# Optimization experiments

Measured on AMD Instinct MI355X. Metric: run time of the kernel, lower is better.

Reference implementation:

```python
import jax, jax.numpy as jnp
import numpy as np

C = 256
NH = 4  # attention heads
G = 8   # groupnorm groups
EPS = 1e-5


def group_norm(x, weight, bias):
    B, Cc, H, W = x.shape
    xg = x.reshape(B, G, Cc // G, H, W)
    mean = xg.mean(axis=(2, 3, 4), keepdims=True)
    var = xg.var(axis=(2, 3, 4), keepdims=True)
    xg = (xg - mean) * jax.lax.rsqrt(var + EPS)
    xn = xg.reshape(B, Cc, H, W)
    return xn * weight[None, :, None, None] + bias[None, :, None, None]


def setup_inputs() -> dict:
    key = jax.random.key(0)
    ks = jax.random.split(key, 7)
    B, H, W = 16, 32, 32
    x = jax.random.normal(ks[0], (B, C, H, W), dtype=jnp.float32)
    n_weight = jnp.ones((C,), dtype=jnp.float32)
    n_bias = jnp.zeros((C,), dtype=jnp.float32)
    qkv_w = jax.random.normal(ks[1], (3 * C, C), dtype=jnp.float32) * (C ** -0.5)
    qkv_b = jnp.zeros((3 * C,), dtype=jnp.float32)
    p_w = jax.random.normal(ks[2], (C, C), dtype=jnp.float32) * (C ** -0.5)
    p_b = jnp.zeros((C,), dtype=jnp.float32)
    return {"x": x, "n_weight": n_weight, "n_bias": n_bias,
            "qkv_w": qkv_w, "qkv_b": qkv_b, "p_w": p_w, "p_b": p_b}


def reference(x, n_weight, n_bias, qkv_w, qkv_b, p_w, p_b):
    B, Cc, H, W = x.shape
    N = H * W
    dh = Cc // NH
    sc = dh ** -0.5
    xn = group_norm(x, n_weight, n_bias)  # [B,C,H,W]
    xn_flat = xn.reshape(B, Cc, N)
    # 1x1 conv == channel matmul
    qkv = jnp.einsum('oc,bcn->bon', qkv_w, xn_flat) + qkv_b[None, :, None]
    qkv = qkv.reshape(B, 3, NH, dh, N)
    q, k, v = qkv[:, 0], qkv[:, 1], qkv[:, 2]  # [B,h,dh,N]
    a = jax.nn.softmax(jnp.einsum('bhci,bhcj->bhij', q, k) * sc, axis=-1)
    o = jnp.einsum('bhij,bhcj->bhci', a, v).reshape(B, Cc, N)
    proj = jnp.einsum('oc,bcn->bon', p_w, o) + p_b[None, :, None]
    return x + proj.reshape(B, Cc, H, W)
```

## Files before the change

kernel.cpp:

```cpp
#include <hip/hip_runtime.h>
#include <math.h>

typedef unsigned short ushort;
typedef unsigned int uint;
typedef __attribute__((ext_vector_type(8))) short bf16x8;
typedef __attribute__((ext_vector_type(4))) float f32x4;

constexpr int Bc  = 16;
constexpr float EPSc = 1e-5f;
constexpr float QSC  = 0.18033688f;

__device__ inline ushort f2bf(float f) {
    uint u = __float_as_uint(f);
    uint r = (u + 0x7fffu + ((u >> 16) & 1u)) >> 16;
    return (ushort)r;
}
__device__ inline uint pack2(float a, float b) {
    return (uint)f2bf(a) | ((uint)f2bf(b) << 16);
}
__device__ __forceinline__ uint cvt2(float a, float b) {
    uint r;
    asm("v_cvt_pk_bf16_f32 %0, %1, %2" : "=v"(r) : "v"(a), "v"(b));
    return r;
}
__device__ __forceinline__ ushort f2bf_fast(float f) {
    uint r;
    asm("v_cvt_pk_bf16_f32 %0, %1, %2" : "=v"(r) : "v"(f), "v"(f));
    return (ushort)r;
}
#if __has_builtin(__builtin_amdgcn_exp2f)
#define EXP2F(x) __builtin_amdgcn_exp2f(x)
#else
#define EXP2F(x) __expf((x) * 0.69314718f)
#endif
__device__ __forceinline__ void gl_lds16(const ushort* g, ushort* l) {
    __builtin_amdgcn_global_load_lds(
        (const __attribute__((address_space(1))) void*)g,
        (__attribute__((address_space(3))) void*)l, 16, 0, 0);
}

__global__ __launch_bounds__(256) void pre_k(
    const float* __restrict__ x, const float* __restrict__ qkvw,
    const float* __restrict__ pw, float* __restrict__ pstats,
    ushort* __restrict__ wqb, ushort* __restrict__ pwb) {
    int blk = blockIdx.x;
    if (blk < 512) {
        int bg = blk >> 2, part = blk & 3;
        const float4* p = (const float4*)(x + (size_t)bg * 32768 + part * 8192);
        float s = 0.f, s2 = 0.f;
        for (int i = threadIdx.x; i < 2048; i += 256) {
            float4 v = p[i];
            s += v.x + v.y + v.z + v.w;
            s2 += v.x*v.x + v.y*v.y + v.z*v.z + v.w*v.w;
        }
        __shared__ float rs[256], rq[256];
        rs[threadIdx.x] = s; rq[threadIdx.x] = s2;
        __syncthreads();
        for (int off = 128; off > 0; off >>= 1) {
            if (threadIdx.x < (unsigned)off) {
                rs[threadIdx.x] += rs[threadIdx.x + off];
                rq[threadIdx.x] += rq[threadIdx.x + off];
            }
            __syncthreads();
        }
        if (threadIdx.x == 0) {
            pstats[blk * 2]     = rs[0];
            pstats[blk * 2 + 1] = rq[0];
        }
    } else {
        int idx = ((blk - 512) * 256 + threadIdx.x) * 4;
        if (idx < 196608) {
            int row = idx >> 8;
            float sc = (row < 256) ? QSC : 1.f;
            float4 v = *(const float4*)&qkvw[idx];
            uint2 u; u.x = cvt2(v.x * sc, v.y * sc); u.y = cvt2(v.z * sc, v.w * sc);
            *(uint2*)&wqb[idx] = u;
        } else {
            int j = idx - 196608;
            float4 v = *(const float4*)&pw[j];
            uint2 u; u.x = cvt2(v.x, v.y); u.y = cvt2(v.z, v.w);
            *(uint2*)&pwb[j] = u;
        }
    }
}

__global__ __launch_bounds__(256) void norm_t_k(
    const float* __restrict__ x, const float* __restrict__ pstats,
    const float* __restrict__ nw, const float* __restrict__ nb,
    ushort* __restrict__ xt) {
    int b = blockIdx.z, ct = blockIdx.y, nt = blockIdx.x;
    __shared__ ushort T[64 * 72];
    int t = threadIdx.x;
    int nn4 = (t & 15) * 4;
#pragma unroll
    for (int p = 0; p < 4; ++p) {
        int cl = (t >> 4) + p * 16;
        int c = ct * 64 + cl;
        int g = c >> 5;
        int base = (b * 8 + g) * 8;
        float s  = (pstats[base] + pstats[base+2]) + (pstats[base+4] + pstats[base+6]);
        float s2 = (pstats[base+1] + pstats[base+3]) + (pstats[base+5] + pstats[base+7]);
        float inv_n = 1.f / 32768.f;
        float mean = s * inv_n;
        float var  = s2 * inv_n - mean * mean;
        float inv  = rsqrtf(var + EPSc);
        float sw = inv * nw[c];
        float sb = nb[c] - mean * sw;
        float4 v = *(const float4*)&x[((size_t)(b * 256 + c)) * 1024 + nt * 64 + nn4];
        T[(nn4 + 0) * 72 + cl] = f2bf_fast(v.x * sw + sb);
        T[(nn4 + 1) * 72 + cl] = f2bf_fast(v.y * sw + sb);
        T[(nn4 + 2) * 72 + cl] = f2bf_fast(v.z * sw + sb);
        T[(nn4 + 3) * 72 + cl] = f2bf_fast(v.w * sw + sb);
    }
    __syncthreads();
#pragma unroll
    for (int p = 0; p < 4; ++p) {
        int nn = (t >> 4) + p * 16;
        int c4 = (t & 15) * 4;
        uint2 w = *(const uint2*)&T[nn * 72 + c4];
        *(uint2*)&xt[((size_t)b * 1024 + nt * 64 + nn) * 256 + ct * 64 + c4] = w;
    }
}

__global__ __launch_bounds__(256, 2) void qkv_gemm_k(
    const ushort* __restrict__ wq, const ushort* __restrict__ xt,
    const float* __restrict__ wb, ushort* __restrict__ qkT,
    ushort* __restrict__ vbuf) {
    int b = blockIdx.z, cy = blockIdx.y, sx = blockIdx.x;
    __shared__ ushort SB[2][2][128 * 64];
    int t = threadIdx.x, lane = t & 63, w = t >> 6;
    int quad = lane >> 4, l15 = lane & 15;
    int wm = w >> 1, wn = w & 1;
    const ushort* wrow = wq + (size_t)cy * 128 * 256;
    const ushort* xrow = xt + ((size_t)b * 1024 + sx * 128) * 256;
    bool tpath = (cy < 4);
    int r0 = t >> 3;
    int cs = (t & 7) ^ (r0 & 7);
    int dst = t * 8;
#pragma unroll
    for (int ps = 0; ps < 4; ++ps) {
        int r = r0 + ps * 32;
        gl_lds16(&wrow[(size_t)r * 256 + cs * 8], &SB[0][0][ps * 2048 + dst]);
        gl_lds16(&xrow[(size_t)r * 256 + cs * 8], &SB[0][1][ps * 2048 + dst]);
    }
    __syncthreads();
    int s0 = quad ^ (l15 & 7);
    f32x4 acc[4][4] = {};
    int cur = 0;
    for (int ki = 0; ki < 4; ++ki) {
        if (ki < 3) {
            int k0 = (ki + 1) * 64, nx = cur ^ 1;
#pragma unroll
            for (int ps = 0; ps < 4; ++ps) {
                int r = r0 + ps * 32;
                gl_lds16(&wrow[(size_t)r * 256 + k0 + cs * 8], &SB[nx][0][ps * 2048 + dst]);
                gl_lds16(&xrow[(size_t)r * 256 + k0 + cs * 8], &SB[nx][1][ps * 2048 + dst]);
            }
        }
        const ushort* Wc = SB[cur][0];
        const ushort* Xc = SB[cur][1];
        const ushort* Am = tpath ? Xc : Wc;
        const ushort* Bn = tpath ? Wc : Xc;
#pragma unroll
        for (int kk = 0; kk < 2; ++kk) {
            int sl = s0 ^ (kk * 4);
            bf16x8 fa[4], fb[4];
#pragma unroll
            for (int mi = 0; mi < 4; ++mi)
                fa[mi] = *(const bf16x8*)&Am[(wm * 64 + mi * 16 + l15) * 64 + sl * 8];
#pragma unroll
            for (int ni = 0; ni < 4; ++ni)
                fb[ni] = *(const bf16x8*)&Bn[(wn * 64 + ni * 16 + l15) * 64 + sl * 8];
#pragma unroll
            for (int mi = 0; mi < 4; ++mi)
#pragma unroll
                for (int ni = 0; ni < 4; ++ni)
                    acc[mi][ni] = __builtin_amdgcn_mfma_f32_16x16x32_bf16(
                        fa[mi], fb[ni], acc[mi][ni], 0, 0, 0);
        }
        __syncthreads();
        cur ^= 1;
    }
    __syncthreads();
    ushort* Tw = ((ushort*)SB) + w * (64 * 72);
    float bsc = (tpath && cy < 2) ? QSC : 1.f;
    if (tpath) {
#pragma unroll
        for (int ni = 0; ni < 4; ++ni) {
            float bias = wb[cy * 128 + wn * 64 + ni * 16 + l15] * bsc;
#pragma unroll
            for (int mi = 0; mi < 4; ++mi)
#pragma unroll
                for (int rr = 0; rr < 4; ++rr)
                    Tw[(mi * 16 + quad * 4 + rr) * 72 + ni * 16 + l15] =
                        f2bf_fast(acc[mi][ni][rr] + bias);
        }
    } else {
#pragma unroll
        for (int mi = 0; mi < 4; ++mi)
#pragma unroll
            for (int rr = 0; rr < 4; ++rr) {
                float bias = wb[cy * 128 + wm * 64 + mi * 16 + quad * 4 + rr];
#pragma unroll
                for (int ni = 0; ni < 4; ++ni)
                    Tw[(mi * 16 + quad * 4 + rr) * 72 + ni * 16 + l15] =
                        f2bf_fast(acc[mi][ni][rr] + bias);
            }
    }
    __asm__ __volatile__("" ::: "memory");
    int row8 = lane >> 3, ch = lane & 7;
#pragma unroll
    for (int p = 0; p < 8; ++p) {
        int row = p * 8 + row8;
        uint4 u = *(const uint4*)&Tw[row * 72 + ch * 8];
        if (tpath) {
            int sp = sx * 128 + wm * 64 + row;
            *(uint4*)&qkT[((size_t)b * 1024 + sp) * 512 + cy * 128 + wn * 64 + ch * 8] = u;
        } else {
            int chanloc = (cy - 4) * 128 + wm * 64 + row;
            *(uint4*)&vbuf[((size_t)b * 256 + chanloc) * 1024 + sx * 128 + wn * 64 + ch * 8] = u;
        }
    }
}

__global__ __launch_bounds__(256, 3) void attn_k(
    const ushort* __restrict__ qkT, const ushort* __restrict__ vbuf,
    ushort* __restrict__ ot) {
    int bh = blockIdx.x;
    int i0 = blockIdx.y * 128;
    int b = bh >> 2, h = bh & 3;
    const ushort* qTb = qkT + (size_t)b * 1024 * 512 + h * 64;
    const ushort* kTb = qTb + 256;
    const ushort* vb  = vbuf + ((size_t)(b * 256 + h * 64)) * 1024;
    __shared__ ushort Ks[2][4096], Vs[2][4096];
    __shared__ ushort Ps[8 * 1152];
    int t = threadIdx.x, lane = t & 63, w = t >> 6;
    int quad = lane >> 4, l15 = lane & 15;
    bf16x8 aq[2][2];
#pragma unroll
    for (int rb = 0; rb < 2; ++rb) {
        const ushort* qr = &qTb[(size_t)(i0 + rb * 64 + w * 16 + l15) * 512];
        aq[rb][0] = *(const bf16x8*)&qr[quad * 8];
        aq[rb][1] = *(const bf16x8*)&qr[32 + quad * 8];
    }
    bf16x8 vones;
#pragma unroll
    for (int i = 0; i < 8; ++i) vones[i] = (short)0x3F80;
    int r0 = t >> 3;
    int cs = (t & 7) ^ (r0 & 7);
    int p0 = quad ^ (l15 & 7);
    int p1 = p0 ^ 4;
    gl_lds16(&kTb[(size_t)r0 * 512 + cs * 8],        &Ks[0][t * 8]);
    gl_lds16(&kTb[(size_t)(r0 + 32) * 512 + cs * 8], &Ks[0][t * 8 + 2048]);
    gl_lds16(&vb[(size_t)r0 * 1024 + cs * 8],        &Vs[0][t * 8]);
    gl_lds16(&vb[(size_t)(r0 + 32) * 1024 + cs * 8], &Vs[0][t * 8 + 2048]);
    __syncthreads();
    f32x4 oacc[2][4] = {};
    f32x4 lacc0 = {0.f, 0.f, 0.f, 0.f};
    f32x4 lacc1 = {0.f, 0.f, 0.f, 0.f};
    ushort* Pw0 = &Ps[(w * 2 + 0) * 1152];
    ushort* Pw1 = &Ps[(w * 2 + 1) * 1152];
    int cur = 0;
    for (int j0 = 0; j0 < 1024; j0 += 64) {
        if (j0 < 960) {
            int jn = j0 + 64, nx = cur ^ 1;
            gl_lds16(&kTb[(size_t)(jn + r0) * 512 + cs * 8],        &Ks[nx][t * 8]);
            gl_lds16(&kTb[(size_t)(jn + r0 + 32) * 512 + cs * 8],   &Ks[nx][t * 8 + 2048]);
            gl_lds16(&vb[(size_t)r0 * 1024 + jn + cs * 8],          &Vs[nx][t * 8]);
            gl_lds16(&vb[(size_t)(r0 + 32) * 1024 + jn + cs * 8],   &Vs[nx][t * 8 + 2048]);
        }
        const ushort* Kc = Ks[cur];
        const ushort* Vc = Vs[cur];
        f32x4 s0[4], s1[4];
        __builtin_amdgcn_s_setprio(1);
#pragma unroll
        for (int jt = 0; jt < 4; ++jt) {
            int row = jt * 16 + l15;
            bf16x8 bk0 = *(const bf16x8*)&Kc[row * 64 + p0 * 8];
            bf16x8 bk1 = *(const bf16x8*)&Kc[row * 64 + p1 * 8];
            f32x4 a = {0.f, 0.f, 0.f, 0.f};
            a = __builtin_amdgcn_mfma_f32_16x16x32_bf16(bk0, aq[0][0], a, 0, 0, 0);
            a = __builtin_amdgcn_mfma_f32_16x16x32_bf16(bk1, aq[0][1], a, 0, 0, 0);
            s0[jt] = a;
            f32x4 c = {0.f, 0.f, 0.f, 0.f};
            c = __builtin_amdgcn_mfma_f32_16x16x32_bf16(bk0, aq[1][0], c, 0, 0, 0);
            c = __builtin_amdgcn_mfma_f32_16x16x32_bf16(bk1, aq[1][1], c, 0, 0, 0);
            s1[jt] = c;
        }
        __builtin_amdgcn_s_setprio(0);
#pragma unroll
        for (int jt = 0; jt < 4; ++jt) {
            int o = l15 * 72 + jt * 16 + quad * 4;
            float e0 = EXP2F(s0[jt][0]), e1 = EXP2F(s0[jt][1]);
            float e2 = EXP2F(s0[jt][2]), e3 = EXP2F(s0[jt][3]);
            uint2 u0; u0.x = cvt2(e0, e1); u0.y = cvt2(e2, e3);
            *(uint2*)&Pw0[o] = u0;
            float f0 = EXP2F(s1[jt][0]), f1 = EXP2F(s1[jt][1]);
            float f2 = EXP2F(s1[jt][2]), f3 = EXP2F(s1[jt][3]);
            uint2 u1; u1.x = cvt2(f0, f1); u1.y = cvt2(f2, f3);
            *(uint2*)&Pw1[o] = u1;
        }
        __asm__ __volatile__("" ::: "memory");
        bf16x8 ap00 = *(const bf16x8*)&Pw0[l15 * 72 + quad * 8];
        bf16x8 ap01 = *(const bf16x8*)&Pw0[l15 * 72 + 32 + quad * 8];
        bf16x8 ap10 = *(const bf16x8*)&Pw1[l15 * 72 + quad * 8];
        bf16x8 ap11 = *(const bf16x8*)&Pw1[l15 * 72 + 32 + quad * 8];
        __builtin_amdgcn_s_setprio(1);
        lacc0 = __builtin_amdgcn_mfma_f32_16x16x32_bf16(ap00, vones, lacc0, 0, 0, 0);
        lacc0 = __builtin_amdgcn_mfma_f32_16x16x32_bf16(ap01, vones, lacc0, 0, 0, 0);
        lacc1 = __builtin_amdgcn_mfma_f32_16x16x32_bf16(ap10, vones, lacc1, 0, 0, 0);
        lacc1 = __builtin_amdgcn_mfma_f32_16x16x32_bf16(ap11, vones, lacc1, 0, 0, 0);
#pragma unroll
        for (int ct = 0; ct < 4; ++ct) {
            int row = ct * 16 + l15;
            bf16x8 bv0 = *(const bf16x8*)&Vc[row * 64 + p0 * 8];
            bf16x8 bv1 = *(const bf16x8*)&Vc[row * 64 + p1 * 8];
            oacc[0][ct] = __builtin_amdgcn_mfma_f32_16x16x32_bf16(ap00, bv0, oacc[0][ct], 0, 0, 0);
            oacc[0][ct] = __builtin_amdgcn_mfma_f32_16x16x32_bf16(ap01, bv1, oacc[0][ct], 0, 0, 0);
            oacc[1][ct] = __builtin_amdgcn_mfma_f32_16x16x32_bf16(ap10, bv0, oacc[1][ct], 0, 0, 0);
            oacc[1][ct] = __builtin_amdgcn_mfma_f32_16x16x32_bf16(ap11, bv1, oacc[1][ct], 0, 0, 0);
        }
        __builtin_amdgcn_s_setprio(0);
        __syncthreads();
        cur ^= 1;
    }
#pragma unroll
    for (int rb = 0; rb < 2; ++rb) {
        f32x4 lv = (rb == 0) ? lacc0 : lacc1;
        float linv[4] = {1.f / lv[0], 1.f / lv[1], 1.f / lv[2], 1.f / lv[3]};
        ushort* Pw = (rb == 0) ? Pw0 : Pw1;
#pragma unroll
        for (int ct = 0; ct < 4; ++ct)
#pragma unroll
            for (int rr = 0; rr < 4; ++rr)
                Pw[(quad * 4 + rr) * 72 + ct * 16 + l15] = f2bf_fast(oacc[rb][ct][rr] * linv[rr]);
        __asm__ __volatile__("" ::: "memory");
#pragma unroll
        for (int p = 0; p < 2; ++p) {
            int row = p * 8 + (lane >> 3), ch = lane & 7;
            uint4 u = *(const uint4*)&Pw[row * 72 + ch * 8];
            *(uint4*)&ot[((size_t)b * 1024 + i0 + rb * 64 + w * 16 + row) * 256 + h * 64 + ch * 8] = u;
        }
    }
}

__global__ __launch_bounds__(256, 3) void proj_k(
    const ushort* __restrict__ pwb, const ushort* __restrict__ ot,
    const float* __restrict__ pb, const float* __restrict__ x,
    float* __restrict__ out) {
    int b = blockIdx.z, cy = blockIdx.y, sx = blockIdx.x;
    __shared__ ushort SB[2][12288];
    int t = threadIdx.x, lane = t & 63, w = t >> 6;
    int quad = lane >> 4, l15 = lane & 15;
    int wm = w >> 1, wn = w & 1;
    const ushort* wrow = pwb + (size_t)cy * 128 * 256;
    const ushort* xrow = ot + ((size_t)b * 1024 + sx * 64) * 256;
    int r0 = t >> 3;
    int cs = (t & 7) ^ (r0 & 7);
    int dst = t * 8;
#pragma unroll
    for (int ps = 0; ps < 4; ++ps)
        gl_lds16(&wrow[(size_t)(r0 + ps * 32) * 256 + cs * 8], &SB[0][ps * 2048 + dst]);
#pragma unroll
    for (int ps = 0; ps < 2; ++ps)
        gl_lds16(&xrow[(size_t)(r0 + ps * 32) * 256 + cs * 8], &SB[0][8192 + ps * 2048 + dst]);
    __syncthreads();
    int p0 = quad ^ (l15 & 7);
    f32x4 acc[4][2] = {};
    int cur = 0;
    for (int ki = 0; ki < 4; ++ki) {
        if (ki < 3) {
            int k0 = (ki + 1) * 64, nx = cur ^ 1;
#pragma unroll
            for (int ps = 0; ps < 4; ++ps)
                gl_lds16(&wrow[(size_t)(r0 + ps * 32) * 256 + k0 + cs * 8], &SB[nx][ps * 2048 + dst]);
#pragma unroll
            for (int ps = 0; ps < 2; ++ps)
                gl_lds16(&xrow[(size_t)(r0 + ps * 32) * 256 + k0 + cs * 8], &SB[nx][8192 + ps * 2048 + dst]);
        }
        const ushort* Wc = &SB[cur][0];
        const ushort* Xc = &SB[cur][8192];
#pragma unroll
        for (int kk = 0; kk < 2; ++kk) {
            int sl = p0 ^ (kk * 4);
            bf16x8 fa[4], fb[2];
#pragma unroll
            for (int mi = 0; mi < 4; ++mi)
                fa[mi] = *(const bf16x8*)&Wc[(wm * 64 + mi * 16 + l15) * 64 + sl * 8];
#pragma unroll
            for (int ni = 0; ni < 2; ++ni)
                fb[ni] = *(const bf16x8*)&Xc[(wn * 32 + ni * 16 + l15) * 64 + sl * 8];
#pragma unroll
            for (int mi = 0; mi < 4; ++mi)
#pragma unroll
                for (int ni = 0; ni < 2; ++ni)
                    acc[mi][ni] = __builtin_amdgcn_mfma_f32_16x16x32_bf16(
                        fa[mi], fb[ni], acc[mi][ni], 0, 0, 0);
        }
        __syncthreads();
        cur ^= 1;
    }
#pragma unroll
    for (int mi = 0; mi < 4; ++mi)
#pragma unroll
        for (int rr = 0; rr < 4; ++rr) {
            int chan = cy * 128 + wm * 64 + mi * 16 + quad * 4 + rr;
            float bias = pb[chan];
#pragma unroll
            for (int ni = 0; ni < 2; ++ni) {
                int sp = sx * 64 + wn * 32 + ni * 16 + l15;
                size_t o = ((size_t)(b * 256 + chan)) * 1024 + sp;
                out[o] = acc[mi][ni][rr] + bias + x[o];
            }
        }
}

extern "C" void kernel_launch(void* const* d_in, const int* in_sizes, int n_in,
                              void* d_out, int out_size, void* d_ws, size_t ws_size,
                              hipStream_t stream) {
    const float* x    = (const float*)d_in[0];
    const float* nw   = (const float*)d_in[1];
    const float* nb   = (const float*)d_in[2];
    const float* qkvw = (const float*)d_in[3];
    const float* qkvb = (const float*)d_in[4];
    const float* pw   = (const float*)d_in[5];
    const float* pb   = (const float*)d_in[6];
    float* out = (float*)d_out;

    float* pstats = (float*)d_ws;
    ushort* base = (ushort*)((char*)d_ws + 4096);
    ushort* xt   = base;
    ushort* wqb  = xt + (size_t)16 * 1024 * 256;
    ushort* pwb  = wqb + 768 * 256;
    ushort* qkT  = pwb + 256 * 256;
    ushort* vbuf = qkT + (size_t)16 * 1024 * 512;
    ushort* ot   = xt;

    pre_k<<<dim3(768), dim3(256), 0, stream>>>(x, qkvw, pw, pstats, wqb, pwb);
    norm_t_k<<<dim3(16, 4, Bc), dim3(256), 0, stream>>>(x, pstats, nw, nb, xt);
    qkv_gemm_k<<<dim3(8, 6, Bc), dim3(256), 0, stream>>>(wqb, xt, qkvb, qkT, vbuf);
    attn_k<<<dim3(64, 8), dim3(256), 0, stream>>>(qkT, vbuf, ot);
    proj_k<<<dim3(16, 2, Bc), dim3(256), 0, stream>>>(pwb, ot, pb, x, out);
}
```

Measured before the change: 128.8 us.

## Fuse groupnorm stats and transpose into one kernel; rewrite attention with 32x32 MFMA

```diff
diff --git a/kernel.cpp b/kernel.cpp
--- a/kernel.cpp
+++ b/kernel.cpp
@@ -5,6 +5,8 @@
 typedef unsigned int uint;
 typedef __attribute__((ext_vector_type(8))) short bf16x8;
 typedef __attribute__((ext_vector_type(4))) float f32x4;
+typedef __attribute__((ext_vector_type(16))) float f32x16;
+typedef __attribute__((ext_vector_type(2))) unsigned uint2v;
 
 constexpr int Bc  = 16;
 constexpr float EPSc = 1e-5f;
@@ -15,9 +17,6 @@
     uint r = (u + 0x7fffu + ((u >> 16) & 1u)) >> 16;
     return (ushort)r;
 }
-__device__ inline uint pack2(float a, float b) {
-    return (uint)f2bf(a) | ((uint)f2bf(b) << 16);
-}
 __device__ __forceinline__ uint cvt2(float a, float b) {
     uint r;
     asm("v_cvt_pk_bf16_f32 %0, %1, %2" : "=v"(r) : "v"(a), "v"(b));
@@ -27,6 +26,14 @@
     uint r;
     asm("v_cvt_pk_bf16_f32 %0, %1, %2" : "=v"(r) : "v"(f), "v"(f));
     return (ushort)r;
+}
+__device__ __forceinline__ uint2v plswap(uint a, uint b) {
+#if __has_builtin(__builtin_amdgcn_permlane32_swap)
+    return __builtin_amdgcn_permlane32_swap(a, b, false, false);
+#else
+    asm volatile("v_permlane32_swap_b32 %0, %1" : "+v"(a), "+v"(b));
+    uint2v r; r.x = a; r.y = b; return r;
+#endif
 }
 #if __has_builtin(__builtin_amdgcn_exp2f)
 #define EXP2F(x) __builtin_amdgcn_exp2f(x)
@@ -39,36 +46,63 @@
         (__attribute__((address_space(3))) void*)l, 16, 0, 0);
 }
 
-__global__ __launch_bounds__(256) void pre_k(
-    const float* __restrict__ x, const float* __restrict__ qkvw,
-    const float* __restrict__ pw, float* __restrict__ pstats,
+__global__ __launch_bounds__(1024, 4) void norm_k(
+    const float* __restrict__ x, const float* __restrict__ nw,
+    const float* __restrict__ nb, const float* __restrict__ qkvw,
+    const float* __restrict__ pw, ushort* __restrict__ xt,
     ushort* __restrict__ wqb, ushort* __restrict__ pwb) {
     int blk = blockIdx.x;
-    if (blk < 512) {
-        int bg = blk >> 2, part = blk & 3;
-        const float4* p = (const float4*)(x + (size_t)bg * 32768 + part * 8192);
+    int t = threadIdx.x;
+    if (blk < 128) {
+        int b = blk >> 3, g = blk & 7;
+        const float* xs = x + ((size_t)(b * 8 + g)) * 32768;
+        const float4* p4 = (const float4*)xs;
         float s = 0.f, s2 = 0.f;
-        for (int i = threadIdx.x; i < 2048; i += 256) {
-            float4 v = p[i];
-            s += v.x + v.y + v.z + v.w;
-            s2 += v.x*v.x + v.y*v.y + v.z*v.z + v.w*v.w;
-        }
-        __shared__ float rs[256], rq[256];
-        rs[threadIdx.x] = s; rq[threadIdx.x] = s2;
+#pragma unroll
+        for (int i = 0; i < 8; ++i) {
+            float4 v = p4[t + i * 1024];
+            s += (v.x + v.y) + (v.z + v.w);
+            s2 += (v.x * v.x + v.y * v.y) + (v.z * v.z + v.w * v.w);
+        }
+#pragma unroll
+        for (int off = 1; off < 64; off <<= 1) {
+            s += __shfl_xor(s, off);
+            s2 += __shfl_xor(s2, off);
+        }
+        __shared__ float rs[16], rq[16], bc[2];
+        int wv = t >> 6, lane = t & 63;
+        if (lane == 0) { rs[wv] = s; rq[wv] = s2; }
         __syncthreads();
-        for (int off = 128; off > 0; off >>= 1) {
-            if (threadIdx.x < (unsigned)off) {
-                rs[threadIdx.x] += rs[threadIdx.x + off];
-                rq[threadIdx.x] += rq[threadIdx.x + off];
-            }
-            __syncthreads();
-        }
-        if (threadIdx.x == 0) {
-            pstats[blk * 2]     = rs[0];
-            pstats[blk * 2 + 1] = rq[0];
+        if (t == 0) {
+            float ts = 0.f, tq = 0.f;
+#pragma unroll
+            for (int i = 0; i < 16; ++i) { ts += rs[i]; tq += rq[i]; }
+            float mean = ts * (1.f / 32768.f);
+            float var  = tq * (1.f / 32768.f) - mean * mean;
+            bc[0] = mean; bc[1] = rsqrtf(var + EPSc);
+        }
+        __syncthreads();
+        float mean = bc[0], inv = bc[1];
+        int n = t;
+        uint w[16];
+#pragma unroll
+        for (int c = 0; c < 32; c += 2) {
+            float w0 = inv * nw[g * 32 + c];
+            float b0 = nb[g * 32 + c] - mean * w0;
+            float w1 = inv * nw[g * 32 + c + 1];
+            float b1 = nb[g * 32 + c + 1] - mean * w1;
+            float v0 = xs[(size_t)c * 1024 + n] * w0 + b0;
+            float v1 = xs[(size_t)(c + 1) * 1024 + n] * w1 + b1;
+            w[c >> 1] = cvt2(v0, v1);
+        }
+        ushort* dst = &xt[((size_t)(b * 1024 + n)) * 256 + g * 32];
+#pragma unroll
+        for (int i = 0; i < 4; ++i) {
+            uint4 u; u.x = w[i*4]; u.y = w[i*4+1]; u.z = w[i*4+2]; u.w = w[i*4+3];
+            *(uint4*)&dst[i * 8] = u;
         }
     } else {
-        int idx = ((blk - 512) * 256 + threadIdx.x) * 4;
+        int idx = ((blk - 128) * 1024 + t) * 4;
         if (idx < 196608) {
             int row = idx >> 8;
             float sc = (row < 256) ? QSC : 1.f;
@@ -81,44 +115,6 @@
             uint2 u; u.x = cvt2(v.x, v.y); u.y = cvt2(v.z, v.w);
             *(uint2*)&pwb[j] = u;
         }
-    }
-}
-
-__global__ __launch_bounds__(256) void norm_t_k(
-    const float* __restrict__ x, const float* __restrict__ pstats,
-    const float* __restrict__ nw, const float* __restrict__ nb,
-    ushort* __restrict__ xt) {
-    int b = blockIdx.z, ct = blockIdx.y, nt = blockIdx.x;
-    __shared__ ushort T[64 * 72];
-    int t = threadIdx.x;
-    int nn4 = (t & 15) * 4;
-#pragma unroll
-    for (int p = 0; p < 4; ++p) {
-        int cl = (t >> 4) + p * 16;
-        int c = ct * 64 + cl;
-        int g = c >> 5;
-        int base = (b * 8 + g) * 8;
-        float s  = (pstats[base] + pstats[base+2]) + (pstats[base+4] + pstats[base+6]);
-        float s2 = (pstats[base+1] + pstats[base+3]) + (pstats[base+5] + pstats[base+7]);
-        float inv_n = 1.f / 32768.f;
-        float mean = s * inv_n;
-        float var  = s2 * inv_n - mean * mean;
-        float inv  = rsqrtf(var + EPSc);
-        float sw = inv * nw[c];
-        float sb = nb[c] - mean * sw;
-        float4 v = *(const float4*)&x[((size_t)(b * 256 + c)) * 1024 + nt * 64 + nn4];
-        T[(nn4 + 0) * 72 + cl] = f2bf_fast(v.x * sw + sb);
-        T[(nn4 + 1) * 72 + cl] = f2bf_fast(v.y * sw + sb);
-        T[(nn4 + 2) * 72 + cl] = f2bf_fast(v.z * sw + sb);
-        T[(nn4 + 3) * 72 + cl] = f2bf_fast(v.w * sw + sb);
-    }
-    __syncthreads();
-#pragma unroll
-    for (int p = 0; p < 4; ++p) {
-        int nn = (t >> 4) + p * 16;
-        int c4 = (t & 15) * 4;
-        uint2 w = *(const uint2*)&T[nn * 72 + c4];
-        *(uint2*)&xt[((size_t)b * 1024 + nt * 64 + nn) * 256 + ct * 64 + c4] = w;
     }
 }
 
@@ -223,7 +219,7 @@
     }
 }
 
-__global__ __launch_bounds__(256, 3) void attn_k(
+__global__ __launch_bounds__(128, 2) void attn_k(
     const ushort* __restrict__ qkT, const ushort* __restrict__ vbuf,
     ushort* __restrict__ ot) {
     int bh = blockIdx.x;
@@ -232,115 +228,129 @@
     const ushort* qTb = qkT + (size_t)b * 1024 * 512 + h * 64;
     const ushort* kTb = qTb + 256;
     const ushort* vb  = vbuf + ((size_t)(b * 256 + h * 64)) * 1024;
-    __shared__ ushort Ks[2][4096], Vs[2][4096];
-    __shared__ ushort Ps[8 * 1152];
-    int t = threadIdx.x, lane = t & 63, w = t >> 6;
-    int quad = lane >> 4, l15 = lane & 15;
-    bf16x8 aq[2][2];
-#pragma unroll
-    for (int rb = 0; rb < 2; ++rb) {
-        const ushort* qr = &qTb[(size_t)(i0 + rb * 64 + w * 16 + l15) * 512];
-        aq[rb][0] = *(const bf16x8*)&qr[quad * 8];
-        aq[rb][1] = *(const bf16x8*)&qr[32 + quad * 8];
-    }
-    bf16x8 vones;
-#pragma unroll
-    for (int i = 0; i < 8; ++i) vones[i] = (short)0x3F80;
-    int r0 = t >> 3;
-    int cs = (t & 7) ^ (r0 & 7);
-    int p0 = quad ^ (l15 & 7);
-    int p1 = p0 ^ 4;
-    gl_lds16(&kTb[(size_t)r0 * 512 + cs * 8],        &Ks[0][t * 8]);
-    gl_lds16(&kTb[(size_t)(r0 + 32) * 512 + cs * 8], &Ks[0][t * 8 + 2048]);
-    gl_lds16(&vb[(size_t)r0 * 1024 + cs * 8],        &Vs[0][t * 8]);
-    gl_lds16(&vb[(size_t)(r0 + 32) * 1024 + cs * 8], &Vs[0][t * 8 + 2048]);
+    __shared__ ushort SM[16384];
+    ushort* Ks0 = SM;
+    ushort* Vs0 = SM + 8192;
+    int t = threadIdx.x, lane = t & 63, wv = t >> 6;
+    int l31 = lane & 31, hf = lane >> 5;
+    int r0 = t >> 3, pc = t & 7;
+#pragma unroll
+    for (int seg = 0; seg < 4; ++seg) {
+        int row = seg * 16 + r0;
+        int c = pc ^ (row & 7);
+        gl_lds16(&kTb[(size_t)row * 512 + c * 8], &Ks0[seg * 1024 + t * 8]);
+        gl_lds16(&vb[(size_t)row * 1024 + c * 8], &Vs0[seg * 1024 + t * 8]);
+    }
+    bf16x8 qf[2][4];
+#pragma unroll
+    for (int ib = 0; ib < 2; ++ib)
+#pragma unroll
+        for (int ks = 0; ks < 4; ++ks)
+            qf[ib][ks] = *(const bf16x8*)
+                &qTb[(size_t)(i0 + wv * 64 + ib * 32 + l31) * 512 + ks * 16 + hf * 8];
     __syncthreads();
-    f32x4 oacc[2][4] = {};
-    f32x4 lacc0 = {0.f, 0.f, 0.f, 0.f};
-    f32x4 lacc1 = {0.f, 0.f, 0.f, 0.f};
-    ushort* Pw0 = &Ps[(w * 2 + 0) * 1152];
-    ushort* Pw1 = &Ps[(w * 2 + 1) * 1152];
+    f32x16 oT00 = {}, oT01 = {}, oT10 = {}, oT11 = {};
+    float lsum0 = 0.f, lsum1 = 0.f;
     int cur = 0;
     for (int j0 = 0; j0 < 1024; j0 += 64) {
+        ushort* Kc = Ks0 + cur * 4096;
+        ushort* Vc = Vs0 + cur * 4096;
         if (j0 < 960) {
-            int jn = j0 + 64, nx = cur ^ 1;
-            gl_lds16(&kTb[(size_t)(jn + r0) * 512 + cs * 8],        &Ks[nx][t * 8]);
-            gl_lds16(&kTb[(size_t)(jn + r0 + 32) * 512 + cs * 8],   &Ks[nx][t * 8 + 2048]);
-            gl_lds16(&vb[(size_t)r0 * 1024 + jn + cs * 8],          &Vs[nx][t * 8]);
-            gl_lds16(&vb[(size_t)(r0 + 32) * 1024 + jn + cs * 8],   &Vs[nx][t * 8 + 2048]);
-        }
-        const ushort* Kc = Ks[cur];
-        const ushort* Vc = Vs[cur];
-        f32x4 s0[4], s1[4];
-        __builtin_amdgcn_s_setprio(1);
-#pragma unroll
-        for (int jt = 0; jt < 4; ++jt) {
-            int row = jt * 16 + l15;
-            bf16x8 bk0 = *(const bf16x8*)&Kc[row * 64 + p0 * 8];
-            bf16x8 bk1 = *(const bf16x8*)&Kc[row * 64 + p1 * 8];
-            f32x4 a = {0.f, 0.f, 0.f, 0.f};
-            a = __builtin_amdgcn_mfma_f32_16x16x32_bf16(bk0, aq[0][0], a, 0, 0, 0);
-            a = __builtin_amdgcn_mfma_f32_16x16x32_bf16(bk1, aq[0][1], a, 0, 0, 0);
-            s0[jt] = a;
-            f32x4 c = {0.f, 0.f, 0.f, 0.f};
-            c = __builtin_amdgcn_mfma_f32_16x16x32_bf16(bk0, aq[1][0], c, 0, 0, 0);
-            c = __builtin_amdgcn_mfma_f32_16x16x32_bf16(bk1, aq[1][1], c, 0, 0, 0);
-            s1[jt] = c;
-        }
-        __builtin_amdgcn_s_setprio(0);
-#pragma unroll
-        for (int jt = 0; jt < 4; ++jt) {
-            int o = l15 * 72 + jt * 16 + quad * 4;
-            float e0 = EXP2F(s0[jt][0]), e1 = EXP2F(s0[jt][1]);
-            float e2 = EXP2F(s0[jt][2]), e3 = EXP2F(s0[jt][3]);
-            uint2 u0; u0.x = cvt2(e0, e1); u0.y = cvt2(e2, e3);
-            *(uint2*)&Pw0[o] = u0;
-            float f0 = EXP2F(s1[jt][0]), f1 = EXP2F(s1[jt][1]);
-            float f2 = EXP2F(s1[jt][2]), f3 = EXP2F(s1[jt][3]);
-            uint2 u1; u1.x = cvt2(f0, f1); u1.y = cvt2(f2, f3);
-            *(uint2*)&Pw1[o] = u1;
-        }
-        __asm__ __volatile__("" ::: "memory");
-        bf16x8 ap00 = *(const bf16x8*)&Pw0[l15 * 72 + quad * 8];
-        bf16x8 ap01 = *(const bf16x8*)&Pw0[l15 * 72 + 32 + quad * 8];
-        bf16x8 ap10 = *(const bf16x8*)&Pw1[l15 * 72 + quad * 8];
-        bf16x8 ap11 = *(const bf16x8*)&Pw1[l15 * 72 + 32 + quad * 8];
-        __builtin_amdgcn_s_setprio(1);
-        lacc0 = __builtin_amdgcn_mfma_f32_16x16x32_bf16(ap00, vones, lacc0, 0, 0, 0);
-        lacc0 = __builtin_amdgcn_mfma_f32_16x16x32_bf16(ap01, vones, lacc0, 0, 0, 0);
-        lacc1 = __builtin_amdgcn_mfma_f32_16x16x32_bf16(ap10, vones, lacc1, 0, 0, 0);
-        lacc1 = __builtin_amdgcn_mfma_f32_16x16x32_bf16(ap11, vones, lacc1, 0, 0, 0);
-#pragma unroll
-        for (int ct = 0; ct < 4; ++ct) {
-            int row = ct * 16 + l15;
-            bf16x8 bv0 = *(const bf16x8*)&Vc[row * 64 + p0 * 8];
-            bf16x8 bv1 = *(const bf16x8*)&Vc[row * 64 + p1 * 8];
-            oacc[0][ct] = __builtin_amdgcn_mfma_f32_16x16x32_bf16(ap00, bv0, oacc[0][ct], 0, 0, 0);
-            oacc[0][ct] = __builtin_amdgcn_mfma_f32_16x16x32_bf16(ap01, bv1, oacc[0][ct], 0, 0, 0);
-            oacc[1][ct] = __builtin_amdgcn_mfma_f32_16x16x32_bf16(ap10, bv0, oacc[1][ct], 0, 0, 0);
-            oacc[1][ct] = __builtin_amdgcn_mfma_f32_16x16x32_bf16(ap11, bv1, oacc[1][ct], 0, 0, 0);
-        }
-        __builtin_amdgcn_s_setprio(0);
+            int nx = cur ^ 1;
+            ushort* Kn = Ks0 + nx * 4096;
+            ushort* Vn = Vs0 + nx * 4096;
+#pragma unroll
+            for (int seg = 0; seg < 4; ++seg) {
+                int row = seg * 16 + r0;
+                int c = pc ^ (row & 7);
+                gl_lds16(&kTb[(size_t)(j0 + 64 + row) * 512 + c * 8], &Kn[seg * 1024 + t * 8]);
+                gl_lds16(&vb[(size_t)row * 1024 + j0 + 64 + c * 8],   &Vn[seg * 1024 + t * 8]);
+            }
+        }
+#pragma unroll
+        for (int jb = 0; jb < 2; ++jb) {
+            f32x16 s0 = {}, s1 = {};
+#pragma unroll
+            for (int ks = 0; ks < 4; ++ks) {
+                int row = jb * 32 + l31;
+                int c = (2 * ks + hf) ^ (row & 7);
+                bf16x8 ak = *(const bf16x8*)&Kc[row * 64 + c * 8];
+                s0 = __builtin_amdgcn_mfma_f32_32x32x16_bf16(ak, qf[0][ks], s0, 0, 0, 0);
+                s1 = __builtin_amdgcn_mfma_f32_32x32x16_bf16(ak, qf[1][ks], s1, 0, 0, 0);
+            }
+            bf16x8 pf[2][2];
+#pragma unroll
+            for (int ib = 0; ib < 2; ++ib) {
+                f32x16 sv = (ib == 0) ? s0 : s1;
+                float e[16];
+#pragma unroll
+                for (int r = 0; r < 16; ++r) e[r] = EXP2F(sv[r]);
+                float ls = ((e[0] + e[1]) + (e[2] + e[3])) + ((e[4] + e[5]) + (e[6] + e[7]))
+                         + ((e[8] + e[9]) + (e[10] + e[11])) + ((e[12] + e[13]) + (e[14] + e[15]));
+                if (ib == 0) lsum0 += ls; else lsum1 += ls;
+                uint w0[4], w1[4];
+#pragma unroll
+                for (int q = 0; q < 4; ++q) {
+                    w0[q] = cvt2(e[q * 4 + 0], e[q * 4 + 1]);
+                    w1[q] = cvt2(e[q * 4 + 2], e[q * 4 + 3]);
+                }
+#pragma unroll
+                for (int s2 = 0; s2 < 2; ++s2) {
+                    uint2v ra = plswap(w0[2 * s2], w0[2 * s2 + 1]);
+                    uint2v rb = plswap(w1[2 * s2], w1[2 * s2 + 1]);
+                    uint4 u; u.x = ra.x; u.y = rb.x; u.z = ra.y; u.w = rb.y;
+                    bf16x8 v; __builtin_memcpy(&v, &u, 16);
+                    pf[ib][s2] = v;
+                }
+            }
+#pragma unroll
+            for (int s2 = 0; s2 < 2; ++s2) {
+#pragma unroll
+                for (int db = 0; db < 2; ++db) {
+                    int row = db * 32 + l31;
+                    int c = (2 * (jb * 2 + s2) + hf) ^ (row & 7);
+                    bf16x8 av = *(const bf16x8*)&Vc[row * 64 + c * 8];
+                    if (db == 0) {
+                        oT00 = __builtin_amdgcn_mfma_f32_32x32x16_bf16(av, pf[0][s2], oT00, 0, 0, 0);
+                        oT01 = __builtin_amdgcn_mfma_f32_32x32x16_bf16(av, pf[1][s2], oT01, 0, 0, 0);
+                    } else {
+                        oT10 = __builtin_amdgcn_mfma_f32_32x32x16_bf16(av, pf[0][s2], oT10, 0, 0, 0);
+                        oT11 = __builtin_amdgcn_mfma_f32_32x32x16_bf16(av, pf[1][s2], oT11, 0, 0, 0);
+                    }
+                }
+            }
+        }
         __syncthreads();
         cur ^= 1;
     }
-#pragma unroll
-    for (int rb = 0; rb < 2; ++rb) {
-        f32x4 lv = (rb == 0) ? lacc0 : lacc1;
-        float linv[4] = {1.f / lv[0], 1.f / lv[1], 1.f / lv[2], 1.f / lv[3]};
-        ushort* Pw = (rb == 0) ? Pw0 : Pw1;
-#pragma unroll
-        for (int ct = 0; ct < 4; ++ct)
-#pragma unroll
-            for (int rr = 0; rr < 4; ++rr)
-                Pw[(quad * 4 + rr) * 72 + ct * 16 + l15] = f2bf_fast(oacc[rb][ct][rr] * linv[rr]);
-        __asm__ __volatile__("" ::: "memory");
-#pragma unroll
-        for (int p = 0; p < 2; ++p) {
-            int row = p * 8 + (lane >> 3), ch = lane & 7;
-            uint4 u = *(const uint4*)&Pw[row * 72 + ch * 8];
-            *(uint4*)&ot[((size_t)b * 1024 + i0 + rb * 64 + w * 16 + row) * 256 + h * 64 + ch * 8] = u;
-        }
+    lsum0 += __shfl_xor(lsum0, 32);
+    lsum1 += __shfl_xor(lsum1, 32);
+    float linv0 = 1.f / lsum0, linv1 = 1.f / lsum1;
+    uint* Os = (uint*)SM + wv * (64 * 33);
+#pragma unroll
+    for (int db = 0; db < 2; ++db)
+#pragma unroll
+        for (int ib = 0; ib < 2; ++ib) {
+            f32x16 ov = (db == 0) ? ((ib == 0) ? oT00 : oT01)
+                                  : ((ib == 0) ? oT10 : oT11);
+            float li = (ib == 0) ? linv0 : linv1;
+            int irow = ib * 32 + l31;
+#pragma unroll
+            for (int q = 0; q < 4; ++q) {
+                uint wa = cvt2(ov[q * 4 + 0] * li, ov[q * 4 + 1] * li);
+                uint wb2 = cvt2(ov[q * 4 + 2] * li, ov[q * 4 + 3] * li);
+                int base = irow * 33 + db * 16 + q * 4 + 2 * hf;
+                Os[base]     = wa;
+                Os[base + 1] = wb2;
+            }
+        }
+    __asm__ __volatile__("" ::: "memory");
+#pragma unroll
+    for (int rr = 0; rr < 8; ++rr) {
+        int irow = (lane >> 3) + rr * 8;
+        const uint* rp = &Os[irow * 33 + (lane & 7) * 4];
+        uint4 u; u.x = rp[0]; u.y = rp[1]; u.z = rp[2]; u.w = rp[3];
+        *(uint4*)&ot[((size_t)b * 1024 + i0 + wv * 64 + irow) * 256 + h * 64 + (lane & 7) * 8] = u;
     }
 }
 
@@ -427,8 +437,7 @@
     const float* pb   = (const float*)d_in[6];
     float* out = (float*)d_out;
 
-    float* pstats = (float*)d_ws;
-    ushort* base = (ushort*)((char*)d_ws + 4096);
+    ushort* base = (ushort*)d_ws;
     ushort* xt   = base;
     ushort* wqb  = xt + (size_t)16 * 1024 * 256;
     ushort* pwb  = wqb + 768 * 256;
@@ -436,9 +445,8 @@
     ushort* vbuf = qkT + (size_t)16 * 1024 * 512;
     ushort* ot   = xt;
 
-    pre_k<<<dim3(768), dim3(256), 0, stream>>>(x, qkvw, pw, pstats, wqb, pwb);
-    norm_t_k<<<dim3(16, 4, Bc), dim3(256), 0, stream>>>(x, pstats, nw, nb, xt);
+    norm_k<<<dim3(192), dim3(1024), 0, stream>>>(x, nw, nb, qkvw, pw, xt, wqb, pwb);
     qkv_gemm_k<<<dim3(8, 6, Bc), dim3(256), 0, stream>>>(wqb, xt, qkvb, qkT, vbuf);
-    attn_k<<<dim3(64, 8), dim3(256), 0, stream>>>(qkT, vbuf, ot);
+    attn_k<<<dim3(64, 8), dim3(128), 0, stream>>>(qkT, vbuf, ot);
     proj_k<<<dim3(16, 2, Bc), dim3(256), 0, stream>>>(pwb, ot, pb, x, out);
 }
```

Measured after the change: 136.4 us. +5.9%, slower.
